# Performance work log

Measured on AMD Instinct MI355X. Metric: run time of the kernel, lower is better.

Reference implementation:

```python
import jax, jax.numpy as jnp
import numpy as np

N = 20000      # nodes (spots)
D = 256        # embed_dim
H = 4          # n_heads
DH = D // H    # head dim
L = 2          # n_layers
E = 320000     # edges (avg degree 16)
K = 48         # static padded-neighbor cap (>= true max degree for this data)
EPS = 1e-5
NEG = -1e30


def setup_inputs() -> dict:
    key = jax.random.key(0)
    ks = jax.random.split(key, 8)
    s = 0.05
    return {
        "expr_embed": jax.random.normal(ks[0], (N, D), jnp.float32),
        "spatial_embed": jax.random.normal(ks[1], (N, D), jnp.float32),
        "in_proj_w": jax.random.normal(ks[2], (L, 3 * D, D), jnp.float32) * s,
        "in_proj_b": jnp.zeros((L, 3 * D), jnp.float32),
        "out_proj_w": jax.random.normal(ks[3], (L, D, D), jnp.float32) * s,
        "out_proj_b": jnp.zeros((L, D), jnp.float32),
        "ffn_w1": jax.random.normal(ks[4], (L, 2 * D, D), jnp.float32) * s,
        "ffn_b1": jnp.zeros((L, 2 * D), jnp.float32),
        "ffn_w2": jax.random.normal(ks[5], (L, D, 2 * D), jnp.float32) * s,
        "ffn_b2": jnp.zeros((L, D), jnp.float32),
        "ln1_g": jnp.ones((L, D), jnp.float32),
        "ln1_b": jnp.zeros((L, D), jnp.float32),
        "ln2_g": jnp.ones((L, D), jnp.float32),
        "ln2_b": jnp.zeros((L, D), jnp.float32),
        "edge_index": jax.random.randint(ks[6], (2, E), 0, N, jnp.int32),
    }


def _build_neighbors(edge_index):
    """Padded neighbor indices (N,K) and key_padding_mask (N,K) (True = pad)."""
    src, tgt = edge_index[0], edge_index[1]
    counts = jnp.zeros((N,), jnp.int32).at[tgt].add(1)
    order = jnp.argsort(tgt)                       # group edges by target
    src_s, tgt_s = src[order], tgt[order]
    offsets = jnp.concatenate([jnp.zeros((1,), jnp.int32),
                               jnp.cumsum(counts)[:-1].astype(jnp.int32)])
    pos = jnp.arange(E, dtype=jnp.int32) - offsets[tgt_s]
    pos = jnp.where(pos < K, pos, K)               # K is out-of-bounds -> dropped
    nbr = jnp.zeros((N, K), jnp.int32).at[tgt_s, pos].set(src_s, mode='drop')
    pad = jnp.ones((N, K), bool).at[tgt_s, pos].set(False, mode='drop')
    iso = counts == 0                              # isolated spots attend to self
    nbr = nbr.at[:, 0].set(jnp.where(iso, jnp.arange(N, dtype=jnp.int32), nbr[:, 0]))
    pad = pad.at[:, 0].set(jnp.where(iso, False, pad[:, 0]))
    return nbr, pad


def _layernorm(x, g, b):
    mu = jnp.mean(x, -1, keepdims=True)
    var = jnp.var(x, -1, keepdims=True)
    return (x - mu) * jax.lax.rsqrt(var + EPS) * g + b


def _forward(expr_embed, spatial_embed, in_proj_w, in_proj_b, out_proj_w,
             out_proj_b, ffn_w1, ffn_b1, ffn_w2, ffn_b2,
             ln1_g, ln1_b, ln2_g, ln2_b, nbr, pad):
    x = expr_embed
    scale = 1.0 / jnp.sqrt(jnp.asarray(DH, x.dtype))
    for i in range(L):
        Wq, Wk, Wv = jnp.split(in_proj_w[i], 3, axis=0)
        bq, bk, bv = jnp.split(in_proj_b[i], 3, axis=0)
        q = (x @ Wq.T + bq).reshape(N, H, DH)
        # project spatial once, gather projected rows (same math as gather-then-project)
        k = (spatial_embed @ Wk.T + bk)[nbr].reshape(N, K, H, DH)
        v = (spatial_embed @ Wv.T + bv)[nbr].reshape(N, K, H, DH)
        scores = jnp.einsum('nhd,nkhd->nhk', q, k) * scale      # (N,H,K)
        scores = jnp.where(pad[:, None, :], NEG, scores)
        attn = jax.nn.softmax(scores, axis=-1)
        ao = jnp.einsum('nhk,nkhd->nhd', attn, v).reshape(N, D)
        ao = ao @ out_proj_w[i].T + out_proj_b[i]
        x = _layernorm(x + ao, ln1_g[i], ln1_b[i])
        h = jax.nn.gelu(x @ ffn_w1[i].T + ffn_b1[i], approximate=False)
        h = h @ ffn_w2[i].T + ffn_b2[i]
        x = _layernorm(x + h, ln2_g[i], ln2_b[i])
    return x


def reference(expr_embed, spatial_embed, in_proj_w, in_proj_b, out_proj_w,
              out_proj_b, ffn_w1, ffn_b1, ffn_w2, ffn_b2,
              ln1_g, ln1_b, ln2_g, ln2_b, edge_index):
    nbr, pad = _build_neighbors(edge_index.astype(jnp.int32))
    return _forward(expr_embed, spatial_embed, in_proj_w, in_proj_b, out_proj_w,
                    out_proj_b, ffn_w1, ffn_b1, ffn_w2, ffn_b2,
                    ln1_g, ln1_b, ln2_g, ln2_b, nbr, pad)
```

## Files before the change

kernel.cpp:

```cpp
#include <hip/hip_runtime.h>

#define N_NODES 20000
#define DIM 256
#define NHEAD 4
#define DHEAD 64
#define NLAYER 2
#define NEDGE 320000
#define KCAP 48
#define NBM64 313
#define NBM128 157

typedef __bf16 v8bf __attribute__((ext_vector_type(8)));
typedef __bf16 v2bf __attribute__((ext_vector_type(2)));
typedef float v4f __attribute__((ext_vector_type(4)));

union LU  { uint4 u; v8bf v; };
union U32 { unsigned u; v2bf v; };

__device__ __forceinline__ unsigned short f2bf(float f) {
    unsigned u = __float_as_uint(f);
    unsigned r = u + 0x7FFFu + ((u >> 16) & 1u);
    return (unsigned short)(r >> 16);
}
__device__ __forceinline__ float bflo(unsigned u) { return __uint_as_float(u << 16); }
__device__ __forceinline__ float bfhi(unsigned u) { return __uint_as_float(u & 0xFFFF0000u); }

__global__ void sniffzero_kernel(const unsigned short* __restrict__ p,
                                 int* __restrict__ flag, int* __restrict__ cnt) {
    if (blockIdx.x == 0) {
        __shared__ int s;
        if (threadIdx.x == 0) s = 0;
        __syncthreads();
        int c = 0;
        for (int i = threadIdx.x; i < 4096; i += 256) {
            unsigned short u = p[i];
            unsigned e = (u >> 7) & 0xFFu;
            if (e == 0xFFu) c++;
            else if (e == 0u && (u & 0x7Fu)) c++;
        }
        atomicAdd(&s, c);
        __syncthreads();
        if (threadIdx.x == 0) flag[0] = (s >= 4) ? 1 : 0;
    } else {
        int i = (blockIdx.x - 1) * 256 + threadIdx.x;
        if (i < N_NODES) cnt[i] = 0;
    }
}

struct ConvBfArgs { const void* src[6]; unsigned short* dst[6]; int n[6]; };

__global__ void conv_bf16_kernel(ConvBfArgs a, const int* __restrict__ flag) {
    const int t  = blockIdx.y;
    const int n  = a.n[t];
    const int i0 = (blockIdx.x * 256 + threadIdx.x) * 4;
    if (i0 >= n) return;
    unsigned short* dst = a.dst[t];
    if (flag[0]) {
        float4 v = *(const float4*)((const float*)a.src[t] + i0);
        ushort4 o;
        o.x = f2bf(v.x); o.y = f2bf(v.y); o.z = f2bf(v.z); o.w = f2bf(v.w);
        *(ushort4*)(dst + i0) = o;
    } else {
        ushort4 u = *(const ushort4*)((const unsigned short*)a.src[t] + i0);
        *(ushort4*)(dst + i0) = u;
    }
}

struct ConvF32Args { const void* src[8]; float* dst[8]; int n[8]; };

__global__ void conv_f32_kernel(ConvF32Args a, const int* __restrict__ flag) {
    const int t  = blockIdx.y;
    const int n  = a.n[t];
    const int i0 = (blockIdx.x * 256 + threadIdx.x) * 4;
    if (i0 >= n) return;
    float* dst = a.dst[t];
    if (flag[0]) {
        float4 v = *(const float4*)((const float*)a.src[t] + i0);
        *(float4*)(dst + i0) = v;
    } else {
        ushort4 u = *(const ushort4*)((const unsigned short*)a.src[t] + i0);
        *(float4*)(dst + i0) = make_float4(bflo(u.x), bflo(u.y), bflo(u.z), bflo(u.w));
    }
}

__global__ void build_nbr_kernel(const int* __restrict__ ei,
                                 int* __restrict__ cnt, int* __restrict__ nbr) {
    int e = blockIdx.x * 256 + threadIdx.x;
    if (e >= NEDGE) return;
    int s = ei[e];
    int t = ei[NEDGE + e];
    int slot = atomicAdd(&cnt[t], 1);
    if (slot < KCAP) nbr[t * KCAP + slot] = s;
}

__device__ __forceinline__ void gemm_body128(
    __bf16 (*As)[72], __bf16 (*Bs)[72],
    const unsigned short* __restrict__ A, const unsigned short* __restrict__ B,
    const float* __restrict__ bias, unsigned short* __restrict__ C,
    int M, int Nc, int Kd, int m0, int nB, int nC, int do_gelu)
{
    const int tid  = threadIdx.x;
    const int wave = tid >> 6;
    const int lane = tid & 63;
    const int wr   = (wave >> 1) * 64;
    const int wc   = (wave & 1) * 64;
    const int lm   = lane & 15;
    const int lk   = (lane >> 4) * 8;
    const int srow = tid >> 3;
    const int scol = (tid & 7) << 3;

    uint4 pa[4], pb[4];
#pragma unroll
    for (int i = 0; i < 4; ++i) {
        int row = srow + i * 32;
        pa[i] = make_uint4(0u, 0u, 0u, 0u);
        if (m0 + row < M)
            pa[i] = *(const uint4*)&A[(size_t)(m0 + row) * Kd + scol];
        pb[i] = *(const uint4*)&B[(size_t)(nB + row) * Kd + scol];
    }

    v4f acc[4][4] = {};

    for (int k0 = 0; k0 < Kd; k0 += 64) {
#pragma unroll
        for (int i = 0; i < 4; ++i) { LU t; t.u = pa[i]; *(v8bf*)&As[srow + i * 32][scol] = t.v; }
#pragma unroll
        for (int i = 0; i < 4; ++i) { LU t; t.u = pb[i]; *(v8bf*)&Bs[srow + i * 32][scol] = t.v; }
        __syncthreads();

        const int kn = k0 + 64;
        if (kn < Kd) {
#pragma unroll
            for (int i = 0; i < 4; ++i) {
                int row = srow + i * 32;
                pa[i] = make_uint4(0u, 0u, 0u, 0u);
                if (m0 + row < M)
                    pa[i] = *(const uint4*)&A[(size_t)(m0 + row) * Kd + kn + scol];
                pb[i] = *(const uint4*)&B[(size_t)(nB + row) * Kd + kn + scol];
            }
        }

#pragma unroll
        for (int ks = 0; ks < 2; ++ks) {
            v8bf af[4], bq[4];
#pragma unroll
            for (int mi = 0; mi < 4; ++mi)
                af[mi] = *(const v8bf*)&As[wr + mi * 16 + lm][ks * 32 + lk];
#pragma unroll
            for (int ni = 0; ni < 4; ++ni)
                bq[ni] = *(const v8bf*)&Bs[wc + ni * 16 + lm][ks * 32 + lk];
#pragma unroll
            for (int mi = 0; mi < 4; ++mi)
#pragma unroll
                for (int ni = 0; ni < 4; ++ni)
                    acc[mi][ni] = __builtin_amdgcn_mfma_f32_16x16x32_bf16(
                        af[mi], bq[ni], acc[mi][ni], 0, 0, 0);
        }
        __syncthreads();
    }

    const int rq = (lane >> 4) << 2;
#pragma unroll
    for (int ni = 0; ni < 4; ++ni) {
        int colb = wc + ni * 16 + lm;
        float bv = bias[nB + colb];
        int colc = nC + colb;
#pragma unroll
        for (int mi = 0; mi < 4; ++mi) {
#pragma unroll
            for (int r = 0; r < 4; ++r) {
                int row = m0 + wr + mi * 16 + rq + r;
                if (row >= M) continue;
                float v = acc[mi][ni][r] + bv;
                if (do_gelu) v = 0.5f * v * (1.0f + erff(v * 0.7071067811865475f));
                C[(size_t)row * Nc + colc] = f2bf(v);
            }
        }
    }
}

__global__ __launch_bounds__(256) void gemm_kernel(
    const unsigned short* __restrict__ A, const unsigned short* __restrict__ B,
    const float* __restrict__ bias, unsigned short* __restrict__ C,
    int M, int Nc, int Kd, int do_gelu)
{
    __shared__ __align__(16) __bf16 As[128][72];
    __shared__ __align__(16) __bf16 Bs[128][72];
    const int n0 = blockIdx.y * 128;
    gemm_body128(As, Bs, A, B, bias, C, M, Nc, Kd, blockIdx.x * 128, n0, n0, do_gelu);
}

__global__ __launch_bounds__(256) void qkv_kernel(
    const unsigned short* __restrict__ x, const unsigned short* __restrict__ spat,
    const unsigned short* __restrict__ W, const float* __restrict__ bias,
    unsigned short* __restrict__ q, unsigned short* __restrict__ kv, int M)
{
    __shared__ __align__(16) __bf16 As[128][72];
    __shared__ __align__(16) __bf16 Bs[128][72];
    const int y = blockIdx.y;
    const unsigned short* A = (y < 2) ? x : spat;
    unsigned short*       C = (y < 2) ? q : kv;
    const int Nc = (y < 2) ? 256 : 512;
    const int nB = y * 128;
    const int nC = (y < 2) ? nB : nB - 256;
    gemm_body128(As, Bs, A, W, bias, C, M, Nc, 256, blockIdx.x * 128, nB, nC, 0);
}

__global__ __launch_bounds__(256) void gemm_ln_kernel(
    const unsigned short* __restrict__ A, const unsigned short* __restrict__ B,
    const float* __restrict__ bias, const unsigned short* __restrict__ xres,
    const float* __restrict__ g, const float* __restrict__ bb,
    unsigned short* __restrict__ xout, void* __restrict__ dout,
    int M, int Kd, int final_out, const int* __restrict__ flag)
{
    __shared__ __align__(16) __bf16 As[64][72];
    __shared__ __align__(16) __bf16 Bs[256][72];
    __shared__ float partS[4][64], partSS[4][64];
    __shared__ float totMu[64], totR[64];

    const int tid  = threadIdx.x;
    const int m0   = blockIdx.x * 64;
    const int wave = tid >> 6;
    const int lane = tid & 63;
    const int wn0  = wave * 64;
    const int lm   = lane & 15;
    const int lk   = (lane >> 4) * 8;
    const int srow = tid >> 3;
    const int scol = (tid & 7) << 3;

    uint4 pa[2], pb[8];
#pragma unroll
    for (int i = 0; i < 2; ++i) {
        int row = srow + i * 32;
        pa[i] = make_uint4(0u, 0u, 0u, 0u);
        if (m0 + row < M)
            pa[i] = *(const uint4*)&A[(size_t)(m0 + row) * Kd + scol];
    }
#pragma unroll
    for (int i = 0; i < 8; ++i) {
        int row = srow + i * 32;
        pb[i] = *(const uint4*)&B[(size_t)row * Kd + scol];
    }

    v4f acc[4][4] = {};

    for (int k0 = 0; k0 < Kd; k0 += 64) {
#pragma unroll
        for (int i = 0; i < 2; ++i) { LU t; t.u = pa[i]; *(v8bf*)&As[srow + i * 32][scol] = t.v; }
#pragma unroll
        for (int i = 0; i < 8; ++i) { LU t; t.u = pb[i]; *(v8bf*)&Bs[srow + i * 32][scol] = t.v; }
        __syncthreads();

        const int kn = k0 + 64;
        if (kn < Kd) {
#pragma unroll
            for (int i = 0; i < 2; ++i) {
                int row = srow + i * 32;
                pa[i] = make_uint4(0u, 0u, 0u, 0u);
                if (m0 + row < M)
                    pa[i] = *(const uint4*)&A[(size_t)(m0 + row) * Kd + kn + scol];
            }
#pragma unroll
            for (int i = 0; i < 8; ++i) {
                int row = srow + i * 32;
                pb[i] = *(const uint4*)&B[(size_t)row * Kd + kn + scol];
            }
        }

#pragma unroll
        for (int ks = 0; ks < 2; ++ks) {
            v8bf af[4], bq[4];
#pragma unroll
            for (int mi = 0; mi < 4; ++mi)
                af[mi] = *(const v8bf*)&As[mi * 16 + lm][ks * 32 + lk];
#pragma unroll
            for (int ni = 0; ni < 4; ++ni)
                bq[ni] = *(const v8bf*)&Bs[wn0 + ni * 16 + lm][ks * 32 + lk];
#pragma unroll
            for (int mi = 0; mi < 4; ++mi)
#pragma unroll
                for (int ni = 0; ni < 4; ++ni)
                    acc[mi][ni] = __builtin_amdgcn_mfma_f32_16x16x32_bf16(
                        af[mi], bq[ni], acc[mi][ni], 0, 0, 0);
        }
        __syncthreads();
    }

    const int rq = (lane >> 4) << 2;
    float gv[4], bv2[4], biasv[4];
#pragma unroll
    for (int ni = 0; ni < 4; ++ni) {
        int col = wn0 + ni * 16 + lm;
        biasv[ni] = bias[col];
        gv[ni]    = g[col];
        bv2[ni]   = bb[col];
    }

    float sl[4][4] = {}, ssl[4][4] = {};
#pragma unroll
    for (int mi = 0; mi < 4; ++mi) {
#pragma unroll
        for (int r = 0; r < 4; ++r) {
            int row = m0 + mi * 16 + rq + r;
#pragma unroll
            for (int ni = 0; ni < 4; ++ni) {
                int col = wn0 + ni * 16 + lm;
                float resv = bflo((unsigned)xres[(size_t)row * DIM + col]);
                float v = acc[mi][ni][r] + biasv[ni] + resv;
                acc[mi][ni][r] = v;
                sl[mi][r]  += v;
                ssl[mi][r] += v * v;
            }
        }
    }
#pragma unroll
    for (int mi = 0; mi < 4; ++mi)
#pragma unroll
        for (int r = 0; r < 4; ++r) {
#pragma unroll
            for (int m = 1; m <= 8; m <<= 1) {
                sl[mi][r]  += __shfl_xor(sl[mi][r],  m, 64);
                ssl[mi][r] += __shfl_xor(ssl[mi][r], m, 64);
            }
        }
    if (lm == 0) {
#pragma unroll
        for (int mi = 0; mi < 4; ++mi)
#pragma unroll
            for (int r = 0; r < 4; ++r) {
                partS[wave][mi * 16 + rq + r]  = sl[mi][r];
                partSS[wave][mi * 16 + rq + r] = ssl[mi][r];
            }
    }
    __syncthreads();
    if (tid < 64) {
        float S = partS[0][tid] + partS[1][tid] + partS[2][tid] + partS[3][tid];
        float SS = partSS[0][tid] + partSS[1][tid] + partSS[2][tid] + partSS[3][tid];
        float mu  = S * (1.0f / DIM);
        float var = SS * (1.0f / DIM) - mu * mu;
        totMu[tid] = mu;
        totR[tid]  = rsqrtf(var + 1e-5f);
    }
    __syncthreads();

#pragma unroll
    for (int mi = 0; mi < 4; ++mi) {
#pragma unroll
        for (int r = 0; r < 4; ++r) {
            int lrow = mi * 16 + rq + r;
            int row  = m0 + lrow;
            if (row >= M) continue;
            float mu = totMu[lrow];
            float rv = totR[lrow];
#pragma unroll
            for (int ni = 0; ni < 4; ++ni) {
                int col = wn0 + ni * 16 + lm;
                float o = (acc[mi][ni][r] - mu) * rv * gv[ni] + bv2[ni];
                if (final_out) {
                    if (flag[0]) ((float*)dout)[(size_t)row * DIM + col] = o;
                    else ((unsigned short*)dout)[(size_t)row * DIM + col] = f2bf(o);
                } else {
                    xout[(size_t)row * DIM + col] = f2bf(o);
                }
            }
        }
    }
}

__global__ __launch_bounds__(256) void attn_kernel(
    const unsigned short* __restrict__ q,
    const unsigned short* __restrict__ kv,
    const int* __restrict__ nbr,
    const int* __restrict__ cnt,
    unsigned short* __restrict__ ao)
{
    const int n    = blockIdx.x;
    const int tid  = threadIdx.x;
    const int h    = tid >> 6;
    const int lane = tid & 63;

    __shared__ float sc[NHEAD][KCAP];
    __shared__ int   nbs[NHEAD][KCAP];

    int deg = cnt[n];
    if (deg > KCAP) deg = KCAP;
    const bool iso = (deg == 0);
    if (iso) deg = 1;

    if (lane < KCAP)
        nbs[h][lane] = (lane < deg) ? (iso ? n : nbr[n * KCAP + lane]) : 0;

    const int sub = lane & 7;
    const int grp = lane >> 3;
    const uint4 qu = *(const uint4*)&q[(size_t)n * DIM + h * DHEAD + sub * 8];
    const unsigned short* kbase = kv + h * DHEAD + sub * 8;
    const int nit = (deg + 7) >> 3;

    const int quarter = lane >> 4;
    const int d0      = (lane & 15) * 4;
    const unsigned short* vbase = kv + 256 + h * DHEAD + d0;
    const int dmax = (deg + 3) & ~3;
    const int npv  = dmax >> 2;

    uint4 ku[6];
#pragma unroll
    for (int it = 0; it < 6; ++it) {
        if (it < nit) {
            int nb = nbs[h][it * 8 + grp];
            ku[it] = *(const uint4*)&kbase[(size_t)nb * 512];
        }
    }
    uint2 vu[8];
#pragma unroll
    for (int it = 0; it < 8; ++it) {
        if (it < npv) {
            int nb = nbs[h][it * 4 + quarter];
            vu[it] = *(const uint2*)&vbase[(size_t)nb * 512];
        }
    }

#pragma unroll
    for (int it = 0; it < 6; ++it) {
        if (it < nit) {
            int j = it * 8 + grp;
            uint4 kz = ku[it];
#if __has_builtin(__builtin_amdgcn_fdot2_f32_bf16)
            U32 a0{qu.x}, a1{qu.y}, a2{qu.z}, a3{qu.w};
            U32 b0{kz.x}, b1{kz.y}, b2{kz.z}, b3{kz.w};
            float p = __builtin_amdgcn_fdot2_f32_bf16(a0.v, b0.v, 0.0f, false);
            p = __builtin_amdgcn_fdot2_f32_bf16(a1.v, b1.v, p, false);
            p = __builtin_amdgcn_fdot2_f32_bf16(a2.v, b2.v, p, false);
            p = __builtin_amdgcn_fdot2_f32_bf16(a3.v, b3.v, p, false);
#else
            float p = bflo(qu.x) * bflo(kz.x);
            p = fmaf(bfhi(qu.x), bfhi(kz.x), p);
            p = fmaf(bflo(qu.y), bflo(kz.y), p);
            p = fmaf(bfhi(qu.y), bfhi(kz.y), p);
            p = fmaf(bflo(qu.z), bflo(kz.z), p);
            p = fmaf(bfhi(qu.z), bfhi(kz.z), p);
            p = fmaf(bflo(qu.w), bflo(kz.w), p);
            p = fmaf(bfhi(qu.w), bfhi(kz.w), p);
#endif
            p += __shfl_xor(p, 1, 64);
            p += __shfl_xor(p, 2, 64);
            p += __shfl_xor(p, 4, 64);
            if (sub == 0 && j < deg) sc[h][j] = p * 0.125f;
        }
    }

    {
        float s  = (lane < deg) ? sc[h][lane] : -1e30f;
        float mx = s;
#pragma unroll
        for (int m = 32; m >= 1; m >>= 1) mx = fmaxf(mx, __shfl_xor(mx, m, 64));
        float e   = (lane < deg) ? __expf(s - mx) : 0.0f;
        float sum = e;
#pragma unroll
        for (int m = 32; m >= 1; m >>= 1) sum += __shfl_xor(sum, m, 64);
        float inv = 1.0f / sum;
        if (lane < KCAP) sc[h][lane] = e * inv;
    }

    {
        float a0 = 0.f, a1 = 0.f, a2 = 0.f, a3 = 0.f;
#pragma unroll
        for (int it = 0; it < 8; ++it) {
            if (it < npv) {
                float w = sc[h][it * 4 + quarter];
                uint2 u = vu[it];
                a0 = fmaf(w, bflo(u.x), a0);
                a1 = fmaf(w, bfhi(u.x), a1);
                a2 = fmaf(w, bflo(u.y), a2);
                a3 = fmaf(w, bfhi(u.y), a3);
            }
        }
        for (int j = 32; j < dmax; j += 4) {
            int j0 = j + quarter;
            int nb = nbs[h][j0];
            uint2 u = *(const uint2*)&vbase[(size_t)nb * 512];
            float w = sc[h][j0];
            a0 = fmaf(w, bflo(u.x), a0);
            a1 = fmaf(w, bfhi(u.x), a1);
            a2 = fmaf(w, bflo(u.y), a2);
            a3 = fmaf(w, bfhi(u.y), a3);
        }
        a0 += __shfl_xor(a0, 16, 64); a0 += __shfl_xor(a0, 32, 64);
        a1 += __shfl_xor(a1, 16, 64); a1 += __shfl_xor(a1, 32, 64);
        a2 += __shfl_xor(a2, 16, 64); a2 += __shfl_xor(a2, 32, 64);
        a3 += __shfl_xor(a3, 16, 64); a3 += __shfl_xor(a3, 32, 64);
        if (lane < 16) {
            uint2 o;
            o.x = (unsigned)f2bf(a0) | ((unsigned)f2bf(a1) << 16);
            o.y = (unsigned)f2bf(a2) | ((unsigned)f2bf(a3) << 16);
            *(uint2*)&ao[(size_t)n * DIM + h * DHEAD + d0] = o;
        }
    }
}

extern "C" void kernel_launch(void* const* d_in, const int* in_sizes, int n_in,
                              void* d_out, int out_size, void* d_ws, size_t ws_size,
                              hipStream_t stream) {
    const int* ei = (const int*)d_in[14];

    char* ws = (char*)d_ws;
    size_t off = 0;
    auto alloc = [&](size_t bytes) -> void* {
        void* p = ws + off;
        off = (off + bytes + 255) & ~(size_t)255;
        return p;
    };

    const int bidx[6] = { 0, 1, 2, 4, 6, 8 };
    const int bnn[6]  = { N_NODES * DIM, N_NODES * DIM,
                          NLAYER * 3 * DIM * DIM, NLAYER * DIM * DIM,
                          NLAYER * 2 * DIM * DIM, NLAYER * DIM * 2 * DIM };
    ConvBfArgs cb;
    unsigned short* canb[6];
    for (int i = 0; i < 6; ++i) {
        canb[i] = (unsigned short*)alloc((size_t)bnn[i] * 2);
        cb.src[i] = d_in[bidx[i]];
        cb.dst[i] = canb[i];
        cb.n[i]   = bnn[i];
    }
    const unsigned short* expr_b = canb[0];
    const unsigned short* spat_b = canb[1];
    const unsigned short* ipw    = canb[2];
    const unsigned short* opw    = canb[3];
    const unsigned short* w1     = canb[4];
    const unsigned short* w2     = canb[5];

    const int fidx[8] = { 3, 5, 7, 9, 10, 11, 12, 13 };
    const int fn[8]   = { NLAYER * 3 * DIM, NLAYER * DIM, NLAYER * 2 * DIM,
                          NLAYER * DIM, NLAYER * DIM, NLAYER * DIM,
                          NLAYER * DIM, NLAYER * DIM };
    ConvF32Args cf;
    float* canf[8];
    for (int i = 0; i < 8; ++i) {
        canf[i] = (float*)alloc((size_t)fn[i] * 4);
        cf.src[i] = d_in[fidx[i]];
        cf.dst[i] = canf[i];
        cf.n[i]   = fn[i];
    }

    unsigned short* x_buf  = (unsigned short*)alloc((size_t)N_NODES * DIM * 2);
    unsigned short* q_buf  = (unsigned short*)alloc((size_t)N_NODES * DIM * 2);
    unsigned short* kv_buf = (unsigned short*)alloc((size_t)N_NODES * 2 * DIM * 2);
    unsigned short* ao_buf = (unsigned short*)alloc((size_t)N_NODES * DIM * 2);
    unsigned short* h_buf  = (unsigned short*)alloc((size_t)N_NODES * 2 * DIM * 2);
    int* cnt  = (int*)alloc((size_t)N_NODES * 4);
    int* nbr  = (int*)alloc((size_t)N_NODES * KCAP * 4);
    int* flag = (int*)alloc(256);

    sniffzero_kernel<<<1 + (N_NODES + 255) / 256, 256, 0, stream>>>(
        (const unsigned short*)d_in[0], flag, cnt);
    conv_bf16_kernel<<<dim3((N_NODES * DIM) / 1024, 6), 256, 0, stream>>>(cb, flag);
    conv_f32_kernel<<<dim3(2, 8), 256, 0, stream>>>(cf, flag);
    build_nbr_kernel<<<(NEDGE + 255) / 256, 256, 0, stream>>>(ei, cnt, nbr);

    for (int i = 0; i < NLAYER; ++i) {
        const unsigned short* Wqkv = ipw + (size_t)i * 3 * DIM * DIM;
        const float*          bqkv = canf[0] + (size_t)i * 3 * DIM;
        const unsigned short* xin  = (i == 0) ? expr_b : x_buf;

        qkv_kernel<<<dim3(NBM128, 6), 256, 0, stream>>>(
            xin, spat_b, Wqkv, bqkv, q_buf, kv_buf, N_NODES);
        attn_kernel<<<N_NODES, 256, 0, stream>>>(q_buf, kv_buf, nbr, cnt, ao_buf);
        gemm_ln_kernel<<<NBM64, 256, 0, stream>>>(
            ao_buf, opw + (size_t)i * DIM * DIM, canf[1] + (size_t)i * DIM,
            xin, canf[4] + (size_t)i * DIM, canf[5] + (size_t)i * DIM,
            x_buf, nullptr, N_NODES, DIM, 0, flag);
        gemm_kernel<<<dim3(NBM128, 4), 256, 0, stream>>>(
            x_buf, w1 + (size_t)i * 2 * DIM * DIM, canf[2] + (size_t)i * 2 * DIM,
            h_buf, N_NODES, 2 * DIM, DIM, 1);
        gemm_ln_kernel<<<NBM64, 256, 0, stream>>>(
            h_buf, w2 + (size_t)i * DIM * 2 * DIM, canf[3] + (size_t)i * DIM,
            x_buf, canf[6] + (size_t)i * DIM, canf[7] + (size_t)i * DIM,
            x_buf, d_out, N_NODES, 2 * DIM, (i == NLAYER - 1) ? 1 : 0, flag);
    }
}
```

Before: 475.2 us.

## Stage GEMM tiles via direct global-to-LDS loads with XOR-swizzled layout

Replaces the register-staged global→LDS copies in all three GEMM kernels with global_load_lds 16-byte direct loads into an unpadded, XOR-swizzled LDS layout, and reads MFMA fragments with the matching swizzle. This drops the register prefetch buffers and padding, shrinking LDS and register use, and adds a min-occupancy hint of 3 blocks per CU for the 128x128 kernels. The register double-buffering (prefetch of the next k-tile during compute) is gone, so load latency is now exposed before each barrier unless occupancy hides it. Out-of-range rows are clamped rather than zeroed, which is harmless because their outputs are masked.

Result: faster. 418.9 us (-11.9%).

```diff
diff --git a/kernel.cpp b/kernel.cpp
--- a/kernel.cpp
+++ b/kernel.cpp
@@ -14,7 +14,6 @@
 typedef __bf16 v2bf __attribute__((ext_vector_type(2)));
 typedef float v4f __attribute__((ext_vector_type(4)));
 
-union LU  { uint4 u; v8bf v; };
 union U32 { unsigned u; v2bf v; };
 
 __device__ __forceinline__ unsigned short f2bf(float f) {
@@ -24,6 +23,34 @@
 }
 __device__ __forceinline__ float bflo(unsigned u) { return __uint_as_float(u << 16); }
 __device__ __forceinline__ float bfhi(unsigned u) { return __uint_as_float(u & 0xFFFF0000u); }
+
+__device__ __forceinline__ void gl2lds(const void* g, void* l) {
+    __builtin_amdgcn_global_load_lds(
+        (const __attribute__((address_space(1))) unsigned int*)g,
+        (__attribute__((address_space(3))) unsigned int*)l, 16, 0, 0);
+}
+
+__device__ __forceinline__ void stage8(const unsigned short* __restrict__ g0,
+                                       size_t stride_e, unsigned short* lds) {
+    const int l = threadIdx.x & 63;
+    const int r = l >> 3;
+    const int c = (l & 7) ^ r;
+    gl2lds(g0 + (size_t)r * stride_e + c * 8, lds);
+}
+__device__ __forceinline__ void stage8c(const unsigned short* __restrict__ base,
+                                        int row0, int rowmax, size_t stride_e,
+                                        int k0, unsigned short* lds) {
+    const int l = threadIdx.x & 63;
+    const int r = l >> 3;
+    const int c = (l & 7) ^ r;
+    int row = row0 + r; row = row > rowmax ? rowmax : row;
+    gl2lds(base + (size_t)row * stride_e + k0 + c * 8, lds);
+}
+
+__device__ __forceinline__ v8bf frag_read(const unsigned short* lds, int row, int col2) {
+    const int bo = row * 128 + (col2 ^ ((row & 7) << 4));
+    return *(const v8bf*)((const char*)lds + bo);
+}
 
 __global__ void sniffzero_kernel(const unsigned short* __restrict__ p,
                                  int* __restrict__ flag, int* __restrict__ cnt) {
@@ -94,7 +121,7 @@
 }
 
 __device__ __forceinline__ void gemm_body128(
-    __bf16 (*As)[72], __bf16 (*Bs)[72],
+    unsigned short* At, unsigned short* Bt,
     const unsigned short* __restrict__ A, const unsigned short* __restrict__ B,
     const float* __restrict__ bias, unsigned short* __restrict__ C,
     int M, int Nc, int Kd, int m0, int nB, int nC, int do_gelu)
@@ -106,49 +133,27 @@
     const int wc   = (wave & 1) * 64;
     const int lm   = lane & 15;
     const int lk   = (lane >> 4) * 8;
-    const int srow = tid >> 3;
-    const int scol = (tid & 7) << 3;
-
-    uint4 pa[4], pb[4];
-#pragma unroll
-    for (int i = 0; i < 4; ++i) {
-        int row = srow + i * 32;
-        pa[i] = make_uint4(0u, 0u, 0u, 0u);
-        if (m0 + row < M)
-            pa[i] = *(const uint4*)&A[(size_t)(m0 + row) * Kd + scol];
-        pb[i] = *(const uint4*)&B[(size_t)(nB + row) * Kd + scol];
-    }
 
     v4f acc[4][4] = {};
 
     for (int k0 = 0; k0 < Kd; k0 += 64) {
 #pragma unroll
-        for (int i = 0; i < 4; ++i) { LU t; t.u = pa[i]; *(v8bf*)&As[srow + i * 32][scol] = t.v; }
-#pragma unroll
-        for (int i = 0; i < 4; ++i) { LU t; t.u = pb[i]; *(v8bf*)&Bs[srow + i * 32][scol] = t.v; }
+        for (int g2 = 0; g2 < 4; ++g2) {
+            const int rr = wave * 32 + g2 * 8;
+            stage8c(A, m0 + rr, M - 1, Kd, k0, At + rr * 64);
+            stage8(B + (size_t)(nB + rr) * Kd + k0, Kd, Bt + rr * 64);
+        }
         __syncthreads();
-
-        const int kn = k0 + 64;
-        if (kn < Kd) {
-#pragma unroll
-            for (int i = 0; i < 4; ++i) {
-                int row = srow + i * 32;
-                pa[i] = make_uint4(0u, 0u, 0u, 0u);
-                if (m0 + row < M)
-                    pa[i] = *(const uint4*)&A[(size_t)(m0 + row) * Kd + kn + scol];
-                pb[i] = *(const uint4*)&B[(size_t)(nB + row) * Kd + kn + scol];
-            }
-        }
 
 #pragma unroll
         for (int ks = 0; ks < 2; ++ks) {
             v8bf af[4], bq[4];
 #pragma unroll
             for (int mi = 0; mi < 4; ++mi)
-                af[mi] = *(const v8bf*)&As[wr + mi * 16 + lm][ks * 32 + lk];
+                af[mi] = frag_read(At, wr + mi * 16 + lm, (ks * 32 + lk) * 2);
 #pragma unroll
             for (int ni = 0; ni < 4; ++ni)
-                bq[ni] = *(const v8bf*)&Bs[wc + ni * 16 + lm][ks * 32 + lk];
+                bq[ni] = frag_read(Bt, wc + ni * 16 + lm, (ks * 32 + lk) * 2);
 #pragma unroll
             for (int mi = 0; mi < 4; ++mi)
 #pragma unroll
@@ -179,31 +184,31 @@
     }
 }
 
-__global__ __launch_bounds__(256) void gemm_kernel(
+__global__ __launch_bounds__(256, 3) void gemm_kernel(
     const unsigned short* __restrict__ A, const unsigned short* __restrict__ B,
     const float* __restrict__ bias, unsigned short* __restrict__ C,
     int M, int Nc, int Kd, int do_gelu)
 {
-    __shared__ __align__(16) __bf16 As[128][72];
-    __shared__ __align__(16) __bf16 Bs[128][72];
+    __shared__ __align__(1024) unsigned short At[128 * 64];
+    __shared__ __align__(1024) unsigned short Bt[128 * 64];
     const int n0 = blockIdx.y * 128;
-    gemm_body128(As, Bs, A, B, bias, C, M, Nc, Kd, blockIdx.x * 128, n0, n0, do_gelu);
-}
-
-__global__ __launch_bounds__(256) void qkv_kernel(
+    gemm_body128(At, Bt, A, B, bias, C, M, Nc, Kd, blockIdx.x * 128, n0, n0, do_gelu);
+}
+
+__global__ __launch_bounds__(256, 3) void qkv_kernel(
     const unsigned short* __restrict__ x, const unsigned short* __restrict__ spat,
     const unsigned short* __restrict__ W, const float* __restrict__ bias,
     unsigned short* __restrict__ q, unsigned short* __restrict__ kv, int M)
 {
-    __shared__ __align__(16) __bf16 As[128][72];
-    __shared__ __align__(16) __bf16 Bs[128][72];
+    __shared__ __align__(1024) unsigned short At[128 * 64];
+    __shared__ __align__(1024) unsigned short Bt[128 * 64];
     const int y = blockIdx.y;
     const unsigned short* A = (y < 2) ? x : spat;
     unsigned short*       C = (y < 2) ? q : kv;
     const int Nc = (y < 2) ? 256 : 512;
     const int nB = y * 128;
     const int nC = (y < 2) ? nB : nB - 256;
-    gemm_body128(As, Bs, A, W, bias, C, M, Nc, 256, blockIdx.x * 128, nB, nC, 0);
+    gemm_body128(At, Bt, A, W, bias, C, M, Nc, 256, blockIdx.x * 128, nB, nC, 0);
 }
 
 __global__ __launch_bounds__(256) void gemm_ln_kernel(
@@ -213,8 +218,8 @@
     unsigned short* __restrict__ xout, void* __restrict__ dout,
     int M, int Kd, int final_out, const int* __restrict__ flag)
 {
-    __shared__ __align__(16) __bf16 As[64][72];
-    __shared__ __align__(16) __bf16 Bs[256][72];
+    __shared__ __align__(1024) unsigned short At[64 * 64];
+    __shared__ __align__(1024) unsigned short Bt[256 * 64];
     __shared__ float partS[4][64], partSS[4][64];
     __shared__ float totMu[64], totR[64];
 
@@ -225,57 +230,31 @@
     const int wn0  = wave * 64;
     const int lm   = lane & 15;
     const int lk   = (lane >> 4) * 8;
-    const int srow = tid >> 3;
-    const int scol = (tid & 7) << 3;
-
-    uint4 pa[2], pb[8];
-#pragma unroll
-    for (int i = 0; i < 2; ++i) {
-        int row = srow + i * 32;
-        pa[i] = make_uint4(0u, 0u, 0u, 0u);
-        if (m0 + row < M)
-            pa[i] = *(const uint4*)&A[(size_t)(m0 + row) * Kd + scol];
-    }
-#pragma unroll
-    for (int i = 0; i < 8; ++i) {
-        int row = srow + i * 32;
-        pb[i] = *(const uint4*)&B[(size_t)row * Kd + scol];
-    }
 
     v4f acc[4][4] = {};
 
     for (int k0 = 0; k0 < Kd; k0 += 64) {
 #pragma unroll
-        for (int i = 0; i < 2; ++i) { LU t; t.u = pa[i]; *(v8bf*)&As[srow + i * 32][scol] = t.v; }
-#pragma unroll
-        for (int i = 0; i < 8; ++i) { LU t; t.u = pb[i]; *(v8bf*)&Bs[srow + i * 32][scol] = t.v; }
+        for (int g2 = 0; g2 < 2; ++g2) {
+            const int rr = wave * 16 + g2 * 8;
+            stage8c(A, m0 + rr, M - 1, Kd, k0, At + rr * 64);
+        }
+#pragma unroll
+        for (int g2 = 0; g2 < 8; ++g2) {
+            const int rr = wave * 64 + g2 * 8;
+            stage8(B + (size_t)rr * Kd + k0, Kd, Bt + rr * 64);
+        }
         __syncthreads();
-
-        const int kn = k0 + 64;
-        if (kn < Kd) {
-#pragma unroll
-            for (int i = 0; i < 2; ++i) {
-                int row = srow + i * 32;
-                pa[i] = make_uint4(0u, 0u, 0u, 0u);
-                if (m0 + row < M)
-                    pa[i] = *(const uint4*)&A[(size_t)(m0 + row) * Kd + kn + scol];
-            }
-#pragma unroll
-            for (int i = 0; i < 8; ++i) {
-                int row = srow + i * 32;
-                pb[i] = *(const uint4*)&B[(size_t)row * Kd + kn + scol];
-            }
-        }
 
 #pragma unroll
         for (int ks = 0; ks < 2; ++ks) {
             v8bf af[4], bq[4];
 #pragma unroll
             for (int mi = 0; mi < 4; ++mi)
-                af[mi] = *(const v8bf*)&As[mi * 16 + lm][ks * 32 + lk];
+                af[mi] = frag_read(At, mi * 16 + lm, (ks * 32 + lk) * 2);
 #pragma unroll
             for (int ni = 0; ni < 4; ++ni)
-                bq[ni] = *(const v8bf*)&Bs[wn0 + ni * 16 + lm][ks * 32 + lk];
+                bq[ni] = frag_read(Bt, wn0 + ni * 16 + lm, (ks * 32 + lk) * 2);
 #pragma unroll
             for (int mi = 0; mi < 4; ++mi)
 #pragma unroll
```
